# Optimization experiments

Measured on AMD Instinct MI355X. Metric: run time of the kernel, lower is better.

The kernel has to match this reference:

```python
import jax, jax.numpy as jnp
import numpy as np

NUM_INSTANCES = 64  # instance ids in [0, 64); id 0 is background and excluded


def _variance_smooth_loss(variances, ins_labels, num_segments):
    # variances: [N, D] float, ins_labels: [N] int
    N, D = variances.shape
    ones = jnp.ones((N,), dtype=variances.dtype)
    counts = jax.ops.segment_sum(ones, ins_labels, num_segments=num_segments)          # [S]
    sums = jax.ops.segment_sum(variances, ins_labels, num_segments=num_segments)       # [S, D]
    safe_counts = jnp.maximum(counts, 1.0)
    means = sums / safe_counts[:, None]                                                # per-instance mean [S, D]
    diff = variances - means[ins_labels]                                               # gather means back [N, D]
    sq = jnp.sum(diff * diff, axis=1)                                                  # [N]
    # per-instance MSE = sum of squared diffs / (K_i * D), matching nn.MSELoss (mean reduction)
    per_ins = jax.ops.segment_sum(sq, ins_labels, num_segments=num_segments) / (safe_counts * D)
    valid = (counts > 0) & (jnp.arange(num_segments) != 0)                             # skip id 0 & absent ids
    return jnp.sum(jnp.where(valid, per_ins, jnp.zeros_like(per_ins)))


def setup_inputs() -> dict:
    key = jax.random.key(0)
    k1, k2 = jax.random.split(key)
    N, D = 4_000_000, 8
    variances = jax.random.normal(k1, (N, D), dtype=jnp.float32)
    ins_labels = jax.random.randint(k2, (N,), 0, NUM_INSTANCES, dtype=jnp.int32)
    return {"variances": variances, "ins_labels": ins_labels}


def reference(variances, ins_labels):
    return _variance_smooth_loss(variances, ins_labels, NUM_INSTANCES)
```

## Files before the change

kernel.cpp:

```cpp
#include <hip/hip_runtime.h>

#define NUM_INST 64
#define BLOCK 256
#define NWAVES 4
#define GRID 2048

typedef float f32x4 __attribute__((ext_vector_type(4)));
typedef short s16x8 __attribute__((ext_vector_type(8)));
typedef int   i32x4 __attribute__((ext_vector_type(4)));

union FragU { i32x4 i; s16x8 s; };

__device__ __forceinline__ unsigned hilo_pack(float v) {
    unsigned h, p;
    asm("v_cvt_pk_bf16_f32 %0, %1, %1" : "=v"(h) : "v"(v));
    const float r = v - __uint_as_float(h << 16);
    asm("v_cvt_pk_bf16_f32 %0, %1, %2" : "=v"(p) : "v"(v), "v"(r));
    return p;
}

__device__ __forceinline__ void chunk_mfma(const int* lbl, float v0, float v1,
                                           float v2, float v3, int c,
                                           f32x4* accS, f32x4* accQ) {
    FragU B1, B2;
    if (c < 8) {
        B1.i = (i32x4){(int)hilo_pack(v0), (int)hilo_pack(v1),
                       (int)hilo_pack(v2), (int)hilo_pack(v3)};
        B2.i = (i32x4){(int)hilo_pack(v0 * v0), (int)hilo_pack(v1 * v1),
                       (int)hilo_pack(v2 * v2), (int)hilo_pack(v3 * v3)};
    } else {
        const int one = (c == 8) ? 0x3F80 : 0;
        B1.i = (i32x4){one, one, one, one};
        B2.i = (i32x4){0, 0, 0, 0};
    }
#pragma unroll
    for (int t = 0; t < 4; ++t) {
        const int m = c + 16 * t;
        FragU A;
        A.i = (i32x4){ lbl[0] == m ? (int)0x3F803F80 : 0,
                       lbl[1] == m ? (int)0x3F803F80 : 0,
                       lbl[2] == m ? (int)0x3F803F80 : 0,
                       lbl[3] == m ? (int)0x3F803F80 : 0 };
        accS[t] = __builtin_amdgcn_mfma_f32_16x16x32_bf16(A.s, B1.s, accS[t], 0, 0, 0);
        accQ[t] = __builtin_amdgcn_mfma_f32_16x16x32_bf16(A.s, B2.s, accQ[t], 0, 0, 0);
    }
}

__global__ __launch_bounds__(BLOCK) void vsl_main(const float* __restrict__ rows,
                                                  const int* __restrict__ labels,
                                                  float* __restrict__ gacc, int n) {
    __shared__ float sm[3072];
    const int tid = threadIdx.x;
    const int w = tid >> 6;
    const int lane = tid & 63;
    const int g = lane >> 4;
    const int c = lane & 15;
    const int cc = c & 7;

    float* const wrow = sm + w * 576;
    int* const wlab = (int*)(wrow + 512);

    f32x4 accS[4], accQ[4];
#pragma unroll
    for (int t = 0; t < 4; ++t) { accS[t] = (f32x4){0,0,0,0}; accQ[t] = (f32x4){0,0,0,0}; }

    const int waveId = blockIdx.x * NWAVES + w;
    const int step = GRID * NWAVES;
    const int nSC = (n + 63) >> 6;
    const int nFullSC = n >> 6;

    f32x4 pr0 = {0,0,0,0}, pr1 = {0,0,0,0};
    int pl = 0;
    int sc = waveId;
    bool stCur = (sc < nFullSC);
    if (stCur) {
        const float* src = rows + (size_t)sc * 512;
        pr0 = *(const f32x4*)(src + lane * 4);
        pr1 = *(const f32x4*)(src + 256 + lane * 4);
        pl = labels[sc * 64 + lane];
    }

    for (; sc < nSC; sc += step) {
        const int scn = sc + step;
        const bool stNext = (scn < nFullSC);

        if (stCur) {
            *(f32x4*)(wrow + lane * 4) = pr0;
            *(f32x4*)(wrow + 256 + lane * 4) = pr1;
            wlab[lane] = pl;
        }
        f32x4 nr0 = {0,0,0,0}, nr1 = {0,0,0,0};
        int nl = 0;
        if (stNext) {
            const float* src = rows + (size_t)scn * 512;
            nr0 = *(const f32x4*)(src + lane * 4);
            nr1 = *(const f32x4*)(src + 256 + lane * 4);
            nl = labels[scn * 64 + lane];
        }

        if (stCur) {
#pragma unroll
            for (int ck = 0; ck < 4; ++ck) {
                const float* rc = wrow + ck * 128;
                const int* lc = wlab + ck * 16;
                const int2 lp = *(const int2*)(lc + 2 * g);
                const int2 lq = *(const int2*)(lc + 2 * g + 8);
                const int lbl[4] = {lp.x, lp.y, lq.x, lq.y};
                const float v0 = rc[g * 16 + cc];
                const float v1 = rc[g * 16 + 8 + cc];
                const float v2 = rc[g * 16 + 64 + cc];
                const float v3 = rc[g * 16 + 72 + cc];
                chunk_mfma(lbl, v0, v1, v2, v3, c, accS, accQ);
            }
        } else {
            const int base = sc << 6;
#pragma unroll
            for (int ck = 0; ck < 4; ++ck) {
                const int r0 = base + ck * 16 + 2 * g;
                int lbl[4];
                float v[4];
#pragma unroll
                for (int q = 0; q < 4; ++q) {
                    const int rq = r0 + (q & 1) + ((q >> 1) << 3);
                    const bool ok = rq < n;
                    const int rs = ok ? rq : 0;
                    v[q] = rows[(size_t)rs * 8 + cc];
                    lbl[q] = ok ? labels[rs] : -1;
                }
                chunk_mfma(lbl, v[0], v[1], v[2], v[3], c, accS, accQ);
            }
        }
        pr0 = nr0; pr1 = nr1; pl = nl; stCur = stNext;
    }

    __syncthreads();
    float* const red = sm;
#pragma unroll
    for (int t = 0; t < 4; ++t) {
#pragma unroll
        for (int rg = 0; rg < 4; ++rg) {
            const int Lr = 16 * t + 4 * g + rg;
            const float vS = accS[t][rg];
            if (c < 10) red[(w * 64 + Lr) * 12 + ((c < 8) ? c : (c == 8 ? 9 : 11))] = vS;
            float sq = accQ[t][rg];
            sq += __shfl_xor(sq, 1, 64);
            sq += __shfl_xor(sq, 2, 64);
            sq += __shfl_xor(sq, 4, 64);
            if (c == 0) red[(w * 64 + Lr) * 12 + 8] = sq;
        }
    }
    __syncthreads();

    for (int j = tid; j < NUM_INST * 10; j += BLOCK) {
        const int Lb = j / 10;
        const int st = j - Lb * 10;
        float v = 0;
#pragma unroll
        for (int ww = 0; ww < NWAVES; ++ww) v += red[(ww * 64 + Lb) * 12 + st];
        atomicAdd(&gacc[j], v);
    }
}

__global__ __launch_bounds__(64) void vsl_final(const float* __restrict__ gacc,
                                                float* __restrict__ out) {
    const int s = threadIdx.x;
    float val = 0.0f;
    const float* base = &gacc[s * 10];
    const float cnt = base[9];
    if (s != 0 && cnt > 0.0f) {
        const float ss = base[8];
        float m2 = 0.0f;
#pragma unroll
        for (int d = 0; d < 8; ++d) {
            const float sd = base[d];
            m2 += sd * sd;
        }
        val = (ss - m2 / cnt) / (cnt * 8.0f);
    }
#pragma unroll
    for (int off = 32; off > 0; off >>= 1) val += __shfl_down(val, off, 64);
    if (s == 0) out[0] = val;
}

extern "C" void kernel_launch(void* const* d_in, const int* in_sizes, int n_in,
                              void* d_out, int out_size, void* d_ws, size_t ws_size,
                              hipStream_t stream) {
    const float* variances = (const float*)d_in[0];
    const int* labels = (const int*)d_in[1];
    const int n = in_sizes[1];
    float* gacc = (float*)d_ws;

    hipMemsetAsync(d_ws, 0, NUM_INST * 10 * sizeof(float), stream);
    vsl_main<<<GRID, BLOCK, 0, stream>>>(variances, labels, gacc, n);
    vsl_final<<<1, 64, 0, stream>>>(gacc, (float*)d_out);
}
```

Measured before the change: 222.7 us.

## Double-buffer row tiles in LDS via direct global-to-LDS loads

Replaces the register-staged prefetch (global load into VGPRs, then ds_write) with global_load_lds DMA into a per-wave double buffer in shared memory. The next super-chunk is issued straight into the alternate buffer, and s_waitcnt vmcnt is used to wait only for the current one. This saves VGPRs and LDS write instructions, and launch bounds now request higher occupancy. The trade-offs are doubled LDS per block and reliance on vmcnt ordering for correctness.

```diff
diff --git a/kernel.cpp b/kernel.cpp
--- a/kernel.cpp
+++ b/kernel.cpp
@@ -4,12 +4,23 @@
 #define BLOCK 256
 #define NWAVES 4
 #define GRID 2048
+#define BUFF 576
 
 typedef float f32x4 __attribute__((ext_vector_type(4)));
 typedef short s16x8 __attribute__((ext_vector_type(8)));
 typedef int   i32x4 __attribute__((ext_vector_type(4)));
 
 union FragU { i32x4 i; s16x8 s; };
+
+typedef __attribute__((address_space(1))) const unsigned GU;
+typedef __attribute__((address_space(3))) unsigned LU;
+
+__device__ __forceinline__ void gload16(const void* g, void* l) {
+    __builtin_amdgcn_global_load_lds((GU*)g, (LU*)l, 16, 0, 0);
+}
+__device__ __forceinline__ void gload4(const void* g, void* l) {
+    __builtin_amdgcn_global_load_lds((GU*)g, (LU*)l, 4, 0, 0);
+}
 
 __device__ __forceinline__ unsigned hilo_pack(float v) {
     unsigned h, p;
@@ -46,10 +57,10 @@
     }
 }
 
-__global__ __launch_bounds__(BLOCK) void vsl_main(const float* __restrict__ rows,
-                                                  const int* __restrict__ labels,
-                                                  float* __restrict__ gacc, int n) {
-    __shared__ float sm[3072];
+__global__ __launch_bounds__(BLOCK, 8) void vsl_main(const float* __restrict__ rows,
+                                                     const int* __restrict__ labels,
+                                                     float* __restrict__ gacc, int n) {
+    __shared__ __align__(16) float sm[NWAVES * 2 * BUFF];
     const int tid = threadIdx.x;
     const int w = tid >> 6;
     const int lane = tid & 63;
@@ -57,8 +68,8 @@
     const int c = lane & 15;
     const int cc = c & 7;
 
-    float* const wrow = sm + w * 576;
-    int* const wlab = (int*)(wrow + 512);
+    float* const buf0 = sm + w * (2 * BUFF);
+    float* const buf1 = buf0 + BUFF;
 
     f32x4 accS[4], accQ[4];
 #pragma unroll
@@ -69,40 +80,36 @@
     const int nSC = (n + 63) >> 6;
     const int nFullSC = n >> 6;
 
-    f32x4 pr0 = {0,0,0,0}, pr1 = {0,0,0,0};
-    int pl = 0;
     int sc = waveId;
     bool stCur = (sc < nFullSC);
     if (stCur) {
         const float* src = rows + (size_t)sc * 512;
-        pr0 = *(const f32x4*)(src + lane * 4);
-        pr1 = *(const f32x4*)(src + 256 + lane * 4);
-        pl = labels[sc * 64 + lane];
-    }
+        gload16(src + (size_t)lane * 4, buf0);
+        gload16(src + 256 + (size_t)lane * 4, buf0 + 256);
+        gload4(labels + (size_t)sc * 64 + lane, buf0 + 512);
+    }
+    bool flip = false;
 
     for (; sc < nSC; sc += step) {
         const int scn = sc + step;
         const bool stNext = (scn < nFullSC);
+        float* const cur = flip ? buf1 : buf0;
+        float* const nxt = flip ? buf0 : buf1;
 
         if (stCur) {
-            *(f32x4*)(wrow + lane * 4) = pr0;
-            *(f32x4*)(wrow + 256 + lane * 4) = pr1;
-            wlab[lane] = pl;
-        }
-        f32x4 nr0 = {0,0,0,0}, nr1 = {0,0,0,0};
-        int nl = 0;
-        if (stNext) {
-            const float* src = rows + (size_t)scn * 512;
-            nr0 = *(const f32x4*)(src + lane * 4);
-            nr1 = *(const f32x4*)(src + 256 + lane * 4);
-            nl = labels[scn * 64 + lane];
-        }
-
-        if (stCur) {
+            if (stNext) {
+                const float* src = rows + (size_t)scn * 512;
+                gload16(src + (size_t)lane * 4, nxt);
+                gload16(src + 256 + (size_t)lane * 4, nxt + 256);
+                gload4(labels + (size_t)scn * 64 + lane, nxt + 512);
+                asm volatile("s_waitcnt vmcnt(3)" ::: "memory");
+            } else {
+                asm volatile("s_waitcnt vmcnt(0)" ::: "memory");
+            }
 #pragma unroll
             for (int ck = 0; ck < 4; ++ck) {
-                const float* rc = wrow + ck * 128;
-                const int* lc = wlab + ck * 16;
+                const float* rc = cur + ck * 128;
+                const int* lc = (const int*)(cur + 512) + ck * 16;
                 const int2 lp = *(const int2*)(lc + 2 * g);
                 const int2 lq = *(const int2*)(lc + 2 * g + 8);
                 const int lbl[4] = {lp.x, lp.y, lq.x, lq.y};
@@ -130,7 +137,8 @@
                 chunk_mfma(lbl, v[0], v[1], v[2], v[3], c, accS, accQ);
             }
         }
-        pr0 = nr0; pr1 = nr1; pl = nl; stCur = stNext;
+        flip = !flip;
+        stCur = stNext;
     }
 
     __syncthreads();
```

Result: slower. 491.9 us (+120.9%).
